# Kernel optimization log

Measured on AMD Instinct MI355X. Metric: run time of the kernel, lower is better.

## Reference

```python
import jax, jax.numpy as jnp
import numpy as np

N_NODES = 100000
N_EDGES = 640000
IN_D = 128
OUT_D = 128


def setup_inputs() -> dict:
    key = jax.random.key(0)
    k_x, k_ei, k_ws, k_wn = jax.random.split(key, 4)
    scale = 1.0 / np.sqrt(IN_D)
    return {
        "x": jax.random.normal(k_x, (N_NODES, IN_D), dtype=jnp.float32),
        "ei": jax.random.randint(k_ei, (2, N_EDGES), 0, N_NODES, dtype=jnp.int64),
        "Ws": jax.random.normal(k_ws, (IN_D, OUT_D), dtype=jnp.float32) * scale,
        "bs": jnp.zeros((OUT_D,), dtype=jnp.float32),
        "Wn": jax.random.normal(k_wn, (IN_D, OUT_D), dtype=jnp.float32) * scale,
        "bn": jnp.zeros((OUT_D,), dtype=jnp.float32),
    }


def reference(x, ei, Ws, bs, Wn, bn):
    # x: [N, in_d], ei: [2, E]
    src, dst = ei[0], ei[1]
    n = x.shape[0]
    # scatter-sum of gathered source features onto destinations
    agg = jax.ops.segment_sum(x[src], dst, num_segments=n)  # [N, in_d]
    # in-degree per destination node
    deg = jax.ops.segment_sum(jnp.ones(src.shape[0], dtype=x.dtype), dst, num_segments=n)  # [N]
    agg = agg / jnp.maximum(deg, 1.0)[:, None]
    # dual linear + relu (dropout is identity in eval)
    return jax.nn.relu(x @ Ws + bs + agg @ Wn + bn)
```

## Files before the change

kernel.cpp:

```cpp
#include <hip/hip_runtime.h>
#include <hip/hip_bf16.h>

#define D 128

typedef __attribute__((ext_vector_type(8))) short short8v;
typedef __attribute__((ext_vector_type(4))) float f32x4;

__device__ __forceinline__ short f2bf(float f) {
    union { float f; unsigned u; } v;
    v.f = f;
    unsigned u = v.u;
    unsigned r = (u + 0x7FFFu + ((u >> 16) & 1u)) >> 16;
    return (short)r;
}

__device__ __forceinline__ float bf2f(unsigned u16) {
    union { unsigned u; float f; } v;
    v.u = u16 << 16;
    return v.f;
}

__device__ __forceinline__ unsigned pkbf2(float lo, float hi) {
    __hip_bfloat162 h = __float22bfloat162_rn(make_float2(lo, hi));
    union { __hip_bfloat162 h; unsigned u; } v;
    v.h = h;
    return v.u;
}

__global__ __launch_bounds__(256) void prep_kernel(const int* __restrict__ dst,
                                                   int* __restrict__ counts, int nE,
                                                   const float* __restrict__ Ws,
                                                   const float* __restrict__ Wn,
                                                   short* __restrict__ WT2,
                                                   const float* __restrict__ x,
                                                   unsigned short* __restrict__ xb,
                                                   int nElem) {
    const int nbE = (nE + 255) >> 8;
    const int b = blockIdx.x;
    if (b < nbE) {
        int e = b * 256 + threadIdx.x;
        if (e < nE) atomicAdd(&counts[dst[e]], 1);
    } else if (b < nbE + 128) {
        int idx = (b - nbE) * 256 + threadIdx.x;
        int nn = idx >> 8;
        int k = idx & 255;
        float v = (k < D) ? Ws[k * D + nn] : Wn[(k - D) * D + nn];
        WT2[idx] = f2bf(v);
    } else {
        int idx = (b - nbE - 128) * 256 + threadIdx.x;
        int base = idx * 8;
        if (base < nElem) {
            float4 lo = *reinterpret_cast<const float4*>(x + base);
            float4 hi = *reinterpret_cast<const float4*>(x + base + 4);
            union { short8v s8; unsigned u[4]; } p;
            p.u[0] = pkbf2(lo.x, lo.y);
            p.u[1] = pkbf2(lo.z, lo.w);
            p.u[2] = pkbf2(hi.x, hi.y);
            p.u[3] = pkbf2(hi.z, hi.w);
            *reinterpret_cast<short8v*>(xb + base) = p.s8;
        }
    }
}

__global__ __launch_bounds__(256) void scan_fused_kernel(int* __restrict__ counts,
                                                         int* __restrict__ bsums,
                                                         int* __restrict__ done,
                                                         int* __restrict__ rowptr,
                                                         int n, int nb) {
    __shared__ int sh[256];
    __shared__ int s_base, s_total;
    const int b = blockIdx.x;
    const int t = threadIdx.x;
    const int i0 = b * 1024 + t * 4;
    int c[4];
    int s = 0;
#pragma unroll
    for (int j = 0; j < 4; ++j) {
        c[j] = (i0 + j < n) ? counts[i0 + j] : 0;
        s += c[j];
    }
    sh[t] = s;
    __syncthreads();
    for (int off = 1; off < 256; off <<= 1) {
        int u = (t >= off) ? sh[t - off] : 0;
        __syncthreads();
        sh[t] += u;
        __syncthreads();
    }
    const int blockAgg = sh[255];
    if (t == 0) {
        bsums[b] = blockAgg;
        __threadfence();
        atomicAdd(done, 1);
        while (atomicAdd(done, 0) < nb) { }
    }
    __syncthreads();
    int xv = (t < nb) ? atomicAdd(&bsums[t], 0) : 0;
    int vb = (t < b) ? xv : 0;
#pragma unroll
    for (int off = 32; off > 0; off >>= 1) {
        vb += __shfl_down(vb, off, 64);
        xv += __shfl_down(xv, off, 64);
    }
    if (t == 0) { s_base = vb; s_total = xv; }
    else if (t == 64 && nb > 64) { atomicAdd(&s_base, 0); }
    __syncthreads();
    if (t == 64) {
        atomicAdd(&s_base, vb);
        atomicAdd(&s_total, xv);
    }
    __syncthreads();
    const int base = s_base;
    int run = base + sh[t] - s;
#pragma unroll
    for (int j = 0; j < 4; ++j) {
        int i = i0 + j;
        if (i < n) {
            rowptr[i] = run;
            counts[i] = run;
            run += c[j];
        }
    }
    if (b == nb - 1 && t == 0) rowptr[n] = s_total;
}

__global__ __launch_bounds__(256) void fill_kernel(const int* __restrict__ src,
                                                   const int* __restrict__ dst,
                                                   int* __restrict__ cursor,
                                                   int* __restrict__ csr, int nE) {
    int e = blockIdx.x * 256 + threadIdx.x;
    if (e < nE) {
        int pos = atomicAdd(&cursor[dst[e]], 1);
        csr[pos] = src[e];
    }
}

__global__ __launch_bounds__(256) void gather_kernel(const int* __restrict__ rowptr,
                                                     const int* __restrict__ csr,
                                                     const unsigned short* __restrict__ xb,
                                                     unsigned* __restrict__ aggOut,
                                                     int n) {
    const int wave = threadIdx.x >> 6;
    const int lane = threadIdx.x & 63;
    const int d0 = blockIdx.x * 8 + wave * 2;
    if (d0 >= n) return;
    const bool has1 = (d0 + 1) < n;

    int iA = rowptr[d0];
    const int endA = rowptr[d0 + 1];
    int iB = has1 ? endA : 0;
    const int endB = has1 ? rowptr[d0 + 2] : 0;
    const int ofs = lane * 2;

    float ax0 = 0.f, ay0 = 0.f, ax1 = 0.f, ay1 = 0.f;

    while (iA + 2 <= endA && iB + 2 <= endB) {
        int a0 = csr[iA], a1 = csr[iA + 1], b0 = csr[iB], b1 = csr[iB + 1];
        unsigned v0 = *reinterpret_cast<const unsigned*>(xb + (size_t)a0 * D + ofs);
        unsigned v1 = *reinterpret_cast<const unsigned*>(xb + (size_t)a1 * D + ofs);
        unsigned w0 = *reinterpret_cast<const unsigned*>(xb + (size_t)b0 * D + ofs);
        unsigned w1 = *reinterpret_cast<const unsigned*>(xb + (size_t)b1 * D + ofs);
        ax0 += bf2f(v0 & 0xffffu) + bf2f(v1 & 0xffffu);
        ay0 += bf2f(v0 >> 16) + bf2f(v1 >> 16);
        ax1 += bf2f(w0 & 0xffffu) + bf2f(w1 & 0xffffu);
        ay1 += bf2f(w0 >> 16) + bf2f(w1 >> 16);
        iA += 2;
        iB += 2;
    }
    while (iA + 2 <= endA) {
        int a0 = csr[iA], a1 = csr[iA + 1];
        unsigned v0 = *reinterpret_cast<const unsigned*>(xb + (size_t)a0 * D + ofs);
        unsigned v1 = *reinterpret_cast<const unsigned*>(xb + (size_t)a1 * D + ofs);
        ax0 += bf2f(v0 & 0xffffu) + bf2f(v1 & 0xffffu);
        ay0 += bf2f(v0 >> 16) + bf2f(v1 >> 16);
        iA += 2;
    }
    while (iB + 2 <= endB) {
        int b0 = csr[iB], b1 = csr[iB + 1];
        unsigned w0 = *reinterpret_cast<const unsigned*>(xb + (size_t)b0 * D + ofs);
        unsigned w1 = *reinterpret_cast<const unsigned*>(xb + (size_t)b1 * D + ofs);
        ax1 += bf2f(w0 & 0xffffu) + bf2f(w1 & 0xffffu);
        ay1 += bf2f(w0 >> 16) + bf2f(w1 >> 16);
        iB += 2;
    }
    if (iA < endA) {
        unsigned v0 = *reinterpret_cast<const unsigned*>(xb + (size_t)csr[iA] * D + ofs);
        ax0 += bf2f(v0 & 0xffffu);
        ay0 += bf2f(v0 >> 16);
    }
    if (iB < endB) {
        unsigned w0 = *reinterpret_cast<const unsigned*>(xb + (size_t)csr[iB] * D + ofs);
        ax1 += bf2f(w0 & 0xffffu);
        ay1 += bf2f(w0 >> 16);
    }

    const int degA = endA - iA + (iA - rowptr[d0]);
    const float invA = 1.0f / fmaxf((float)(endA - rowptr[d0]), 1.0f);
    aggOut[(size_t)d0 * D + lane] = pkbf2(ax0 * invA, ay0 * invA);
    (void)degA;
    if (has1) {
        const float invB = 1.0f / fmaxf((float)(endB - endA), 1.0f);
        aggOut[(size_t)(d0 + 1) * D + lane] = pkbf2(ax1 * invB, ay1 * invB);
    }
}

__global__ __launch_bounds__(256) void gemm_kernel(const unsigned short* __restrict__ xb,
                                                   const short* __restrict__ WT2,
                                                   const float* __restrict__ bs,
                                                   const float* __restrict__ bn,
                                                   const unsigned* __restrict__ aggIn,
                                                   float* __restrict__ out,
                                                   int n, int nStrips) {
    const int wave = threadIdx.x >> 6;
    const int lane = threadIdx.x & 63;
    const int lrow = lane & 15;
    const int q = lane >> 4;
    const int ko = q * 8;

    short8v b[2][8];
#pragma unroll
    for (int j = 0; j < 2; ++j) {
        const short* __restrict__ wp = WT2 + (size_t)((wave * 2 + j) * 16 + lrow) * 256 + ko;
#pragma unroll
        for (int ks = 0; ks < 8; ++ks)
            b[j][ks] = *reinterpret_cast<const short8v*>(wp + ks * 32);
    }
    float4 bias[2];
#pragma unroll
    for (int j = 0; j < 2; ++j) {
        const int cb = (wave * 2 + j) * 16 + q * 4;
        float4 v1 = *reinterpret_cast<const float4*>(bs + cb);
        float4 v2 = *reinterpret_cast<const float4*>(bn + cb);
        bias[j] = make_float4(v1.x + v2.x, v1.y + v2.y, v1.z + v2.z, v1.w + v2.w);
    }

    for (int strip = blockIdx.x; strip < nStrips; strip += gridDim.x) {
        const int m0 = strip * 16;

        short8v a[8];
        const unsigned short* __restrict__ xr = xb + (size_t)(m0 + lrow) * D + ko;
        const unsigned* __restrict__ ar = aggIn + (size_t)(m0 + lrow) * D;
#pragma unroll
        for (int ks = 0; ks < 4; ++ks) {
            a[ks] = *reinterpret_cast<const short8v*>(xr + ks * 32);
            union { uint4 u4; short8v s8; } cv;
            cv.u4 = *reinterpret_cast<const uint4*>(ar + q * 4 + ks * 16);
            a[4 + ks] = cv.s8;
        }

        __syncthreads();

        f32x4 acc[2];
        acc[0] = (f32x4){0.f, 0.f, 0.f, 0.f};
        acc[1] = (f32x4){0.f, 0.f, 0.f, 0.f};
#pragma unroll
        for (int j = 0; j < 2; ++j)
#pragma unroll
            for (int ks = 0; ks < 8; ++ks)
                acc[j] = __builtin_amdgcn_mfma_f32_16x16x32_bf16(b[j][ks], a[ks], acc[j], 0, 0, 0);

        const size_t rb = (size_t)(m0 + lrow) * D;
#pragma unroll
        for (int j = 0; j < 2; ++j) {
            const int cb = (wave * 2 + j) * 16 + q * 4;
            float4 o;
            o.x = fmaxf(acc[j][0] + bias[j].x, 0.f);
            o.y = fmaxf(acc[j][1] + bias[j].y, 0.f);
            o.z = fmaxf(acc[j][2] + bias[j].z, 0.f);
            o.w = fmaxf(acc[j][3] + bias[j].w, 0.f);
            *reinterpret_cast<float4*>(out + rb + cb) = o;
        }
    }
}

extern "C" void kernel_launch(void* const* d_in, const int* in_sizes, int n_in,
                              void* d_out, int out_size, void* d_ws, size_t ws_size,
                              hipStream_t stream) {
    const float* x  = (const float*)d_in[0];
    const int*   ei = (const int*)d_in[1];
    const float* Ws = (const float*)d_in[2];
    const float* bs = (const float*)d_in[3];
    const float* Wn = (const float*)d_in[4];
    const float* bn = (const float*)d_in[5];
    float* out = (float*)d_out;

    const int n  = in_sizes[0] / D;
    const int nE = in_sizes[1] / 2;
    const int* src = ei;
    const int* dst = ei + nE;
    const int nb = (n + 1023) / 1024;
    const int nElem = n * D;

    unsigned short* xb = (unsigned short*)d_ws;
    short* WT2   = (short*)(xb + (size_t)nElem);
    int*   counts = (int*)(WT2 + (size_t)D * 256);
    int*   bsums  = counts + n;
    int*   done   = bsums + 128;
    int*   rowptr = done + 1;
    int*   csr    = rowptr + n + 1;

    const int nbE = (nE + 255) / 256;
    const int nXb = (nElem / 8 + 255) / 256;

    hipMemsetAsync(counts, 0, (size_t)(n + 129) * sizeof(int), stream);
    prep_kernel<<<nbE + 128 + nXb, 256, 0, stream>>>(dst, counts, nE, Ws, Wn, WT2, x, xb, nElem);
    scan_fused_kernel<<<nb, 256, 0, stream>>>(counts, bsums, done, rowptr, n, nb);
    fill_kernel<<<(nE + 255) / 256, 256, 0, stream>>>(src, dst, counts, csr, nE);

    gather_kernel<<<(n + 7) / 8, 256, 0, stream>>>(rowptr, csr, xb, (unsigned*)out, n);

    const int nStrips = (n + 15) / 16;
    const int gGrid = nStrips < 2048 ? nStrips : 2048;
    gemm_kernel<<<gGrid, 256, 0, stream>>>(xb, WT2, bs, bn, (const unsigned*)out, out, n, nStrips);
}
```

Measured before the change: 165.6 us.

## Fuse CSR build into persistent kernel, unroll gather, double-buffer GEMM loads

Merges the count, conversion, scan and fill kernels into one persistent 1024-block kernel that synchronises its phases with global atomic barriers, removing two launches. The gather loop is unrolled to four neighbours per step to keep more loads in flight. When workspace allows, the aggregate goes to a separate compact buffer so the GEMM can skip its in-place sync, and the GEMM prefetches the next strip's operands while computing the current one. The grid-wide barriers assume all 1024 blocks are resident at once, and the persistent build loops give up some parallelism compared with one-thread-per-element launches.

```diff
diff --git a/kernel.cpp b/kernel.cpp
--- a/kernel.cpp
+++ b/kernel.cpp
@@ -27,110 +27,94 @@
     return v.u;
 }
 
-__global__ __launch_bounds__(256) void prep_kernel(const int* __restrict__ dst,
-                                                   int* __restrict__ counts, int nE,
-                                                   const float* __restrict__ Ws,
-                                                   const float* __restrict__ Wn,
-                                                   short* __restrict__ WT2,
-                                                   const float* __restrict__ x,
-                                                   unsigned short* __restrict__ xb,
-                                                   int nElem) {
-    const int nbE = (nE + 255) >> 8;
-    const int b = blockIdx.x;
-    if (b < nbE) {
-        int e = b * 256 + threadIdx.x;
-        if (e < nE) atomicAdd(&counts[dst[e]], 1);
-    } else if (b < nbE + 128) {
-        int idx = (b - nbE) * 256 + threadIdx.x;
-        int nn = idx >> 8;
-        int k = idx & 255;
-        float v = (k < D) ? Ws[k * D + nn] : Wn[(k - D) * D + nn];
-        WT2[idx] = f2bf(v);
-    } else {
-        int idx = (b - nbE - 128) * 256 + threadIdx.x;
-        int base = idx * 8;
-        if (base < nElem) {
-            float4 lo = *reinterpret_cast<const float4*>(x + base);
-            float4 hi = *reinterpret_cast<const float4*>(x + base + 4);
-            union { short8v s8; unsigned u[4]; } p;
-            p.u[0] = pkbf2(lo.x, lo.y);
-            p.u[1] = pkbf2(lo.z, lo.w);
-            p.u[2] = pkbf2(hi.x, hi.y);
-            p.u[3] = pkbf2(hi.z, hi.w);
-            *reinterpret_cast<short8v*>(xb + base) = p.s8;
-        }
-    }
-}
-
-__global__ __launch_bounds__(256) void scan_fused_kernel(int* __restrict__ counts,
-                                                         int* __restrict__ bsums,
-                                                         int* __restrict__ done,
-                                                         int* __restrict__ rowptr,
-                                                         int n, int nb) {
+__global__ __launch_bounds__(256, 4) void build_kernel(
+    const int* __restrict__ src, const int* __restrict__ dst, int nE,
+    const float* __restrict__ Ws, const float* __restrict__ Wn,
+    short* __restrict__ WT2,
+    const float* __restrict__ x, unsigned short* __restrict__ xb, int nElem,
+    int* __restrict__ counts, int* __restrict__ bsums, int* __restrict__ barCnt,
+    int* __restrict__ rowptr, int* __restrict__ csr, int n, int nb) {
+    const int b = blockIdx.x, t = threadIdx.x, G = gridDim.x;
+    const int gtid = b * 256 + t, gsz = G * 256;
+
+    for (int e = gtid; e < nE; e += gsz) atomicAdd(&counts[dst[e]], 1);
+    for (int i8 = gtid; i8 < nElem / 8; i8 += gsz) {
+        const int base = i8 * 8;
+        float4 lo = *reinterpret_cast<const float4*>(x + base);
+        float4 hi = *reinterpret_cast<const float4*>(x + base + 4);
+        union { short8v s8; unsigned u[4]; } p;
+        p.u[0] = pkbf2(lo.x, lo.y);
+        p.u[1] = pkbf2(lo.z, lo.w);
+        p.u[2] = pkbf2(hi.x, hi.y);
+        p.u[3] = pkbf2(hi.z, hi.w);
+        *reinterpret_cast<short8v*>(xb + base) = p.s8;
+    }
+    for (int idx = gtid; idx < 256 * D; idx += gsz) {
+        const int nn = idx >> 8, k = idx & 255;
+        WT2[idx] = f2bf((k < D) ? Ws[k * D + nn] : Wn[(k - D) * D + nn]);
+    }
+    __syncthreads();
+    if (t == 0) {
+        atomicAdd(barCnt, 1);
+        while (atomicAdd(barCnt, 0) < G) __builtin_amdgcn_s_sleep(2);
+    }
+    __syncthreads();
+
     __shared__ int sh[256];
-    __shared__ int s_base, s_total;
-    const int b = blockIdx.x;
-    const int t = threadIdx.x;
+    __shared__ int red[8];
     const int i0 = b * 1024 + t * 4;
-    int c[4];
-    int s = 0;
-#pragma unroll
-    for (int j = 0; j < 4; ++j) {
-        c[j] = (i0 + j < n) ? counts[i0 + j] : 0;
-        s += c[j];
-    }
-    sh[t] = s;
-    __syncthreads();
-    for (int off = 1; off < 256; off <<= 1) {
-        int u = (t >= off) ? sh[t - off] : 0;
+    int c0 = 0, c1 = 0, c2 = 0, c3 = 0, s = 0;
+    if (b < nb) {
+        c0 = (i0 + 0 < n) ? atomicAdd(&counts[i0 + 0], 0) : 0;
+        c1 = (i0 + 1 < n) ? atomicAdd(&counts[i0 + 1], 0) : 0;
+        c2 = (i0 + 2 < n) ? atomicAdd(&counts[i0 + 2], 0) : 0;
+        c3 = (i0 + 3 < n) ? atomicAdd(&counts[i0 + 3], 0) : 0;
+        s = c0 + c1 + c2 + c3;
+        sh[t] = s;
         __syncthreads();
-        sh[t] += u;
+        for (int off = 1; off < 256; off <<= 1) {
+            int u = (t >= off) ? sh[t - off] : 0;
+            __syncthreads();
+            sh[t] += u;
+            __syncthreads();
+        }
+        if (t == 0) atomicExch(&bsums[b], sh[255]);
+    }
+    __syncthreads();
+    if (t == 0) {
+        atomicAdd(barCnt, 1);
+        while (atomicAdd(barCnt, 0) < 2 * G) __builtin_amdgcn_s_sleep(2);
+    }
+    __syncthreads();
+
+    if (b < nb) {
+        int xv = (t < nb) ? atomicAdd(&bsums[t], 0) : 0;
+        int vb = (t < b) ? xv : 0;
+#pragma unroll
+        for (int off = 32; off > 0; off >>= 1) {
+            vb += __shfl_down(vb, off, 64);
+            xv += __shfl_down(xv, off, 64);
+        }
+        if ((t & 63) == 0) { red[t >> 6] = vb; red[4 + (t >> 6)] = xv; }
         __syncthreads();
-    }
-    const int blockAgg = sh[255];
+        const int base = red[0] + red[1] + red[2] + red[3];
+        const int total = red[4] + red[5] + red[6] + red[7];
+        int run = base + sh[t] - s;
+        if (i0 + 0 < n) { rowptr[i0 + 0] = run; atomicExch(&counts[i0 + 0], run); run += c0; }
+        if (i0 + 1 < n) { rowptr[i0 + 1] = run; atomicExch(&counts[i0 + 1], run); run += c1; }
+        if (i0 + 2 < n) { rowptr[i0 + 2] = run; atomicExch(&counts[i0 + 2], run); run += c2; }
+        if (i0 + 3 < n) { rowptr[i0 + 3] = run; atomicExch(&counts[i0 + 3], run); run += c3; }
+        if (b == 0 && t == 0) rowptr[n] = total;
+    }
+    __syncthreads();
     if (t == 0) {
-        bsums[b] = blockAgg;
-        __threadfence();
-        atomicAdd(done, 1);
-        while (atomicAdd(done, 0) < nb) { }
-    }
-    __syncthreads();
-    int xv = (t < nb) ? atomicAdd(&bsums[t], 0) : 0;
-    int vb = (t < b) ? xv : 0;
-#pragma unroll
-    for (int off = 32; off > 0; off >>= 1) {
-        vb += __shfl_down(vb, off, 64);
-        xv += __shfl_down(xv, off, 64);
-    }
-    if (t == 0) { s_base = vb; s_total = xv; }
-    else if (t == 64 && nb > 64) { atomicAdd(&s_base, 0); }
-    __syncthreads();
-    if (t == 64) {
-        atomicAdd(&s_base, vb);
-        atomicAdd(&s_total, xv);
-    }
-    __syncthreads();
-    const int base = s_base;
-    int run = base + sh[t] - s;
-#pragma unroll
-    for (int j = 0; j < 4; ++j) {
-        int i = i0 + j;
-        if (i < n) {
-            rowptr[i] = run;
-            counts[i] = run;
-            run += c[j];
-        }
-    }
-    if (b == nb - 1 && t == 0) rowptr[n] = s_total;
-}
-
-__global__ __launch_bounds__(256) void fill_kernel(const int* __restrict__ src,
-                                                   const int* __restrict__ dst,
-                                                   int* __restrict__ cursor,
-                                                   int* __restrict__ csr, int nE) {
-    int e = blockIdx.x * 256 + threadIdx.x;
-    if (e < nE) {
-        int pos = atomicAdd(&cursor[dst[e]], 1);
+        atomicAdd(barCnt, 1);
+        while (atomicAdd(barCnt, 0) < 3 * G) __builtin_amdgcn_s_sleep(2);
+    }
+    __syncthreads();
+
+    for (int e = gtid; e < nE; e += gsz) {
+        int pos = atomicAdd(&counts[dst[e]], 1);
         csr[pos] = src[e];
     }
 }
@@ -139,78 +123,81 @@
                                                      const int* __restrict__ csr,
                                                      const unsigned short* __restrict__ xb,
                                                      unsigned* __restrict__ aggOut,
-                                                     int n) {
+                                                     int aggStride, int n) {
     const int wave = threadIdx.x >> 6;
     const int lane = threadIdx.x & 63;
     const int d0 = blockIdx.x * 8 + wave * 2;
     if (d0 >= n) return;
     const bool has1 = (d0 + 1) < n;
 
-    int iA = rowptr[d0];
+    const int begA = rowptr[d0];
     const int endA = rowptr[d0 + 1];
-    int iB = has1 ? endA : 0;
+    const int begB = has1 ? endA : 0;
     const int endB = has1 ? rowptr[d0 + 2] : 0;
     const int ofs = lane * 2;
-
     float ax0 = 0.f, ay0 = 0.f, ax1 = 0.f, ay1 = 0.f;
-
-    while (iA + 2 <= endA && iB + 2 <= endB) {
-        int a0 = csr[iA], a1 = csr[iA + 1], b0 = csr[iB], b1 = csr[iB + 1];
-        unsigned v0 = *reinterpret_cast<const unsigned*>(xb + (size_t)a0 * D + ofs);
-        unsigned v1 = *reinterpret_cast<const unsigned*>(xb + (size_t)a1 * D + ofs);
-        unsigned w0 = *reinterpret_cast<const unsigned*>(xb + (size_t)b0 * D + ofs);
-        unsigned w1 = *reinterpret_cast<const unsigned*>(xb + (size_t)b1 * D + ofs);
-        ax0 += bf2f(v0 & 0xffffu) + bf2f(v1 & 0xffffu);
-        ay0 += bf2f(v0 >> 16) + bf2f(v1 >> 16);
-        ax1 += bf2f(w0 & 0xffffu) + bf2f(w1 & 0xffffu);
-        ay1 += bf2f(w0 >> 16) + bf2f(w1 >> 16);
-        iA += 2;
-        iB += 2;
-    }
-    while (iA + 2 <= endA) {
-        int a0 = csr[iA], a1 = csr[iA + 1];
-        unsigned v0 = *reinterpret_cast<const unsigned*>(xb + (size_t)a0 * D + ofs);
-        unsigned v1 = *reinterpret_cast<const unsigned*>(xb + (size_t)a1 * D + ofs);
-        ax0 += bf2f(v0 & 0xffffu) + bf2f(v1 & 0xffffu);
-        ay0 += bf2f(v0 >> 16) + bf2f(v1 >> 16);
-        iA += 2;
-    }
-    while (iB + 2 <= endB) {
-        int b0 = csr[iB], b1 = csr[iB + 1];
-        unsigned w0 = *reinterpret_cast<const unsigned*>(xb + (size_t)b0 * D + ofs);
-        unsigned w1 = *reinterpret_cast<const unsigned*>(xb + (size_t)b1 * D + ofs);
-        ax1 += bf2f(w0 & 0xffffu) + bf2f(w1 & 0xffffu);
-        ay1 += bf2f(w0 >> 16) + bf2f(w1 >> 16);
-        iB += 2;
-    }
-    if (iA < endA) {
-        unsigned v0 = *reinterpret_cast<const unsigned*>(xb + (size_t)csr[iA] * D + ofs);
-        ax0 += bf2f(v0 & 0xffffu);
-        ay0 += bf2f(v0 >> 16);
-    }
-    if (iB < endB) {
-        unsigned w0 = *reinterpret_cast<const unsigned*>(xb + (size_t)csr[iB] * D + ofs);
-        ax1 += bf2f(w0 & 0xffffu);
-        ay1 += bf2f(w0 >> 16);
-    }
-
-    const int degA = endA - iA + (iA - rowptr[d0]);
-    const float invA = 1.0f / fmaxf((float)(endA - rowptr[d0]), 1.0f);
-    aggOut[(size_t)d0 * D + lane] = pkbf2(ax0 * invA, ay0 * invA);
-    (void)degA;
+    int iA = begA, iB = begB;
+
+#define GLD(sidx) (*reinterpret_cast<const unsigned*>(xb + (size_t)(sidx) * D + ofs))
+    while (iA + 4 <= endA && iB + 4 <= endB) {
+        int a0 = csr[iA], a1 = csr[iA + 1], a2 = csr[iA + 2], a3 = csr[iA + 3];
+        int b0 = csr[iB], b1 = csr[iB + 1], b2 = csr[iB + 2], b3 = csr[iB + 3];
+        unsigned va0 = GLD(a0), va1 = GLD(a1), va2 = GLD(a2), va3 = GLD(a3);
+        unsigned vb0 = GLD(b0), vb1 = GLD(b1), vb2 = GLD(b2), vb3 = GLD(b3);
+        ax0 += (bf2f(va0 & 0xffffu) + bf2f(va1 & 0xffffu)) +
+               (bf2f(va2 & 0xffffu) + bf2f(va3 & 0xffffu));
+        ay0 += (bf2f(va0 >> 16) + bf2f(va1 >> 16)) + (bf2f(va2 >> 16) + bf2f(va3 >> 16));
+        ax1 += (bf2f(vb0 & 0xffffu) + bf2f(vb1 & 0xffffu)) +
+               (bf2f(vb2 & 0xffffu) + bf2f(vb3 & 0xffffu));
+        ay1 += (bf2f(vb0 >> 16) + bf2f(vb1 >> 16)) + (bf2f(vb2 >> 16) + bf2f(vb3 >> 16));
+        iA += 4;
+        iB += 4;
+    }
+    while (iA + 4 <= endA) {
+        int a0 = csr[iA], a1 = csr[iA + 1], a2 = csr[iA + 2], a3 = csr[iA + 3];
+        unsigned va0 = GLD(a0), va1 = GLD(a1), va2 = GLD(a2), va3 = GLD(a3);
+        ax0 += (bf2f(va0 & 0xffffu) + bf2f(va1 & 0xffffu)) +
+               (bf2f(va2 & 0xffffu) + bf2f(va3 & 0xffffu));
+        ay0 += (bf2f(va0 >> 16) + bf2f(va1 >> 16)) + (bf2f(va2 >> 16) + bf2f(va3 >> 16));
+        iA += 4;
+    }
+    while (iB + 4 <= endB) {
+        int b0 = csr[iB], b1 = csr[iB + 1], b2 = csr[iB + 2], b3 = csr[iB + 3];
+        unsigned vb0 = GLD(b0), vb1 = GLD(b1), vb2 = GLD(b2), vb3 = GLD(b3);
+        ax1 += (bf2f(vb0 & 0xffffu) + bf2f(vb1 & 0xffffu)) +
+               (bf2f(vb2 & 0xffffu) + bf2f(vb3 & 0xffffu));
+        ay1 += (bf2f(vb0 >> 16) + bf2f(vb1 >> 16)) + (bf2f(vb2 >> 16) + bf2f(vb3 >> 16));
+        iB += 4;
+    }
+    while (iA < endA) {
+        unsigned v = GLD(csr[iA]);
+        ax0 += bf2f(v & 0xffffu);
+        ay0 += bf2f(v >> 16);
+        ++iA;
+    }
+    while (iB < endB) {
+        unsigned v = GLD(csr[iB]);
+        ax1 += bf2f(v & 0xffffu);
+        ay1 += bf2f(v >> 16);
+        ++iB;
+    }
+#undef GLD
+
+    const float invA = 1.0f / fmaxf((float)(endA - begA), 1.0f);
+    aggOut[(size_t)d0 * aggStride + lane] = pkbf2(ax0 * invA, ay0 * invA);
     if (has1) {
-        const float invB = 1.0f / fmaxf((float)(endB - endA), 1.0f);
-        aggOut[(size_t)(d0 + 1) * D + lane] = pkbf2(ax1 * invB, ay1 * invB);
-    }
-}
-
+        const float invB = 1.0f / fmaxf((float)(endB - begB), 1.0f);
+        aggOut[(size_t)(d0 + 1) * aggStride + lane] = pkbf2(ax1 * invB, ay1 * invB);
+    }
+}
+
+template <bool INPLACE>
 __global__ __launch_bounds__(256) void gemm_kernel(const unsigned short* __restrict__ xb,
                                                    const short* __restrict__ WT2,
                                                    const float* __restrict__ bs,
                                                    const float* __restrict__ bn,
-                                                   const unsigned* __restrict__ aggIn,
-                                                   float* __restrict__ out,
-                                                   int n, int nStrips) {
+                                                   const unsigned* aggIn, int aggStride,
+                                                   float* __restrict__ out, int nStrips) {
     const int wave = threadIdx.x >> 6;
     const int lane = threadIdx.x & 63;
     const int lrow = lane & 15;
@@ -234,32 +221,34 @@
         bias[j] = make_float4(v1.x + v2.x, v1.y + v2.y, v1.z + v2.z, v1.w + v2.w);
     }
 
-    for (int strip = blockIdx.x; strip < nStrips; strip += gridDim.x) {
-        const int m0 = strip * 16;
-
-        short8v a[8];
-        const unsigned short* __restrict__ xr = xb + (size_t)(m0 + lrow) * D + ko;
-        const unsigned* __restrict__ ar = aggIn + (size_t)(m0 + lrow) * D;
+    const int stride = gridDim.x;
+
+    auto loadA = [&](int strip, short8v* ax, uint4* ag) {
+        const unsigned short* __restrict__ xr = xb + (size_t)(strip * 16 + lrow) * D + ko;
+        const unsigned* __restrict__ ar = aggIn + (size_t)(strip * 16 + lrow) * aggStride;
 #pragma unroll
         for (int ks = 0; ks < 4; ++ks) {
-            a[ks] = *reinterpret_cast<const short8v*>(xr + ks * 32);
-            union { uint4 u4; short8v s8; } cv;
-            cv.u4 = *reinterpret_cast<const uint4*>(ar + q * 4 + ks * 16);
-            a[4 + ks] = cv.s8;
-        }
-
-        __syncthreads();
-
+            ax[ks] = *reinterpret_cast<const short8v*>(xr + ks * 32);
+            ag[ks] = *reinterpret_cast<const uint4*>(ar + q * 4 + ks * 16);
+        }
+    };
+
+    auto compute = [&](int strip, const short8v* ax, const uint4* ag) {
         f32x4 acc[2];
         acc[0] = (f32x4){0.f, 0.f, 0.f, 0.f};
         acc[1] = (f32x4){0.f, 0.f, 0.f, 0.f};
 #pragma unroll
-        for (int j = 0; j < 2; ++j)
-#pragma unroll
-            for (int ks = 0; ks < 8; ++ks)
-                acc[j] = __builtin_amdgcn_mfma_f32_16x16x32_bf16(b[j][ks], a[ks], acc[j], 0, 0, 0);
-
-        const size_t rb = (size_t)(m0 + lrow) * D;
+        for (int j = 0; j < 2; ++j) {
+#pragma unroll
+            for (int ks = 0; ks < 4; ++ks) {
+                union { uint4 u4; short8v s8; } cv;
+                cv.u4 = ag[ks];
+                acc[j] = __builtin_amdgcn_mfma_f32_16x16x32_bf16(b[j][ks], ax[ks], acc[j], 0, 0, 0);
+                acc[j] = __builtin_amdgcn_mfma_f32_16x16x32_bf16(b[j][ks + 4], cv.s8, acc[j], 0, 0, 0);
+            }
+        }
+        if (INPLACE) __syncthreads();
+        const size_t rb = (size_t)(strip * 16 + lrow) * D;
 #pragma unroll
         for (int j = 0; j < 2; ++j) {
             const int cb = (wave * 2 + j) * 16 + q * 4;
@@ -269,6 +258,22 @@
             o.z = fmaxf(acc[j][2] + bias[j].z, 0.f);
             o.w = fmaxf(acc[j][3] + bias[j].w, 0.f);
             *reinterpret_cast<float4*>(out + rb + cb) = o;
+        }
+    };
+
+    short8v axA[4], axB[4];
+    uint4 agA[4], agB[4];
+    int strip = blockIdx.x;
+    if (strip >= nStrips) return;
+    loadA(strip, axA, agA);
+    for (; strip < nStrips; strip += 2 * stride) {
+        const int s1 = strip + stride;
+        if (s1 < nStrips) loadA(s1, axB, agB);
+        compute(strip, axA, agA);
+        if (s1 < nStrips) {
+            const int s2 = s1 + stride;
+            if (s2 < nStrips) loadA(s2, axA, agA);
+            compute(s1, axB, agB);
         }
     }
 }
@@ -291,25 +296,33 @@
     const int nb = (n + 1023) / 1024;
     const int nElem = n * D;
 
-    unsigned short* xb = (unsigned short*)d_ws;
-    short* WT2   = (short*)(xb + (size_t)nElem);
-    int*   counts = (int*)(WT2 + (size_t)D * 256);
-    int*   bsums  = counts + n;
-    int*   done   = bsums + 128;
-    int*   rowptr = done + 1;
-    int*   csr    = rowptr + n + 1;
-
-    const int nbE = (nE + 255) / 256;
-    const int nXb = (nElem / 8 + 255) / 256;
-
-    hipMemsetAsync(counts, 0, (size_t)(n + 129) * sizeof(int), stream);
-    prep_kernel<<<nbE + 128 + nXb, 256, 0, stream>>>(dst, counts, nE, Ws, Wn, WT2, x, xb, nElem);
-    scan_fused_kernel<<<nb, 256, 0, stream>>>(counts, bsums, done, rowptr, n, nb);
-    fill_kernel<<<(nE + 255) / 256, 256, 0, stream>>>(src, dst, counts, csr, nE);
-
-    gather_kernel<<<(n + 7) / 8, 256, 0, stream>>>(rowptr, csr, xb, (unsigned*)out, n);
+    char* w = (char*)d_ws;
+    unsigned short* xb = (unsigned short*)w;  w += (size_t)nElem * 2;
+    short* WT2   = (short*)w;                 w += (size_t)256 * D * 2;
+    int* counts  = (int*)w;                   w += (size_t)n * 4;
+    int* bsums   = (int*)w;                   w += 1024 * 4;
+    int* barCnt  = (int*)w;                   w += 16;
+    int* rowptr  = (int*)w;                   w += (size_t)(n + 1) * 4;
+    int* csr     = (int*)w;                   w += (size_t)nE * 4;
+    size_t off = (size_t)(w - (char*)d_ws);
+    off = (off + 15) & ~(size_t)15;
+    unsigned short* aggb = (unsigned short*)((char*)d_ws + off);
+    const bool sep = (off + (size_t)nElem * 2) <= ws_size;
+
+    hipMemsetAsync(counts, 0, (size_t)(n + 1024 + 4) * sizeof(int), stream);
+
+    build_kernel<<<1024, 256, 0, stream>>>(src, dst, nE, Ws, Wn, WT2, x, xb, nElem,
+                                           counts, bsums, barCnt, rowptr, csr, n, nb);
+
+    unsigned* aggPtr = sep ? (unsigned*)aggb : (unsigned*)out;
+    const int aggStride = sep ? (D / 2) : D;
+    gather_kernel<<<(n + 7) / 8, 256, 0, stream>>>(rowptr, csr, xb, aggPtr, aggStride, n);
 
     const int nStrips = (n + 15) / 16;
-    const int gGrid = nStrips < 2048 ? nStrips : 2048;
-    gemm_kernel<<<gGrid, 256, 0, stream>>>(xb, WT2, bs, bn, (const unsigned*)out, out, n, nStrips);
-}
+    if (sep)
+        gemm_kernel<false><<<2048, 256, 0, stream>>>(xb, WT2, bs, bn, (const unsigned*)aggb,
+                                                     aggStride, out, nStrips);
+    else
+        gemm_kernel<true><<<2048, 256, 0, stream>>>(xb, WT2, bs, bn, (const unsigned*)out,
+                                                    aggStride, out, nStrips);
+}
```

New measurement: 259.3 us. 56.6% more time.
